# Optimization experiments

Measured on AMD Instinct MI355X. Metric: run time of the kernel, lower is better.

## Reference

```python
import jax, jax.numpy as jnp
import numpy as np

NEG = 10000.0


def setup_inputs() -> dict:
    key0 = jax.random.key(0)
    k1, k2, k3, k4 = jax.random.split(key0, 4)
    B, S, D = 4, 4096, 64
    query = jax.random.normal(k1, (B, S, D), dtype=jnp.float32)
    key = jax.random.normal(k2, (B, S, D), dtype=jnp.float32)
    value = jax.random.normal(k3, (B, S, D), dtype=jnp.float32)
    mask = jax.random.randint(k4, (B, S), 0, 2, dtype=jnp.int32)
    return {"query": query, "key": key, "value": value, "mask": mask}


def reference(query, key, value, mask):
    B, Sq, D = query.shape
    Sk = key.shape[1]
    # scaled scores: [B, Sq, Sk]
    e = jnp.einsum("bqd,bkd->bqk", query, key) / jnp.sqrt(jnp.asarray(D, query.dtype))
    # history_only (causal) additive mask: penalize positions where key idx > query idx
    causal = (jnp.arange(Sk)[None, :] > jnp.arange(Sq)[:, None]).astype(query.dtype)
    e = e - NEG * causal[None, :, :]
    # padding mask on keys: [B, 1, Sk]
    e = e - NEG * (1.0 - mask.astype(query.dtype))[:, None, :]
    attn = jax.nn.softmax(e, axis=-1)
    return jnp.einsum("bqk,bkd->bqd", attn, value)
```

## Files before the change

kernel.cpp:

```cpp
#include <hip/hip_runtime.h>

typedef __attribute__((ext_vector_type(8))) short  bf16x8;
typedef __attribute__((ext_vector_type(4))) float  f32x4;

#define S_LEN 4096
#define DH    64
#define NEGF  10000.0f

__device__ __forceinline__ unsigned short f2bf(float f) {
  unsigned u = __float_as_uint(f);
  u += 0x7FFF + ((u >> 16) & 1);
  return (unsigned short)(u >> 16);
}

__device__ __forceinline__ bf16x8 pack8(float4 a, float4 b) {
  bf16x8 r;
  r[0] = (short)f2bf(a.x); r[1] = (short)f2bf(a.y);
  r[2] = (short)f2bf(a.z); r[3] = (short)f2bf(a.w);
  r[4] = (short)f2bf(b.x); r[5] = (short)f2bf(b.y);
  r[6] = (short)f2bf(b.z); r[7] = (short)f2bf(b.w);
  return r;
}

__device__ __forceinline__ int swz(int row, int colb) {
  return (row << 7) + (colb ^ ((row & 7) << 4));
}

__global__ __launch_bounds__(1024, 1)
void attn_fwd(const float* __restrict__ Q, const float* __restrict__ K,
              const float* __restrict__ V, const int* __restrict__ Msk,
              float* __restrict__ O) {
  __shared__ __align__(16) unsigned char smem[98304];
  __shared__ int sfb;
  unsigned char* smK  = smem;
  unsigned char* smVt = smem + 32768;
  unsigned char* smP  = smem + 65536;

  const int tid  = threadIdx.x;
  const int lane = tid & 63;
  const int wid  = tid >> 6;
  const int g    = wid >> 2;
  const int r    = wid & 3;
  const int p    = lane & 15;
  const int h    = lane >> 4;

  const int b  = blockIdx.x >> 6;
  const int qt = blockIdx.x & 63;
  const int q0 = qt << 6;

  const float* Qb = Q + ((size_t)b * S_LEN) * DH;
  const float* Kb = K + ((size_t)b * S_LEN) * DH;
  const float* Vb = V + ((size_t)b * S_LEN) * DH;
  const int*   Mb = Msk + b * S_LEN;

  if (tid == 0) sfb = S_LEN;
  __syncthreads();
  {
    int loc = S_LEN;
    for (int k = tid; k < S_LEN; k += 1024)
      if (Mb[k]) { loc = k; break; }
    if (loc < S_LEN) atomicMin(&sfb, loc);
  }
  __syncthreads();
  const int fb = sfb;

  bf16x8 qf[2];
  {
    const float* qp = Qb + (size_t)(q0 + g * 16 + p) * DH + h * 8;
    const float4* q4a = (const float4*)(qp);
    const float4* q4b = (const float4*)(qp + 32);
    qf[0] = pack8(q4a[0], q4a[1]);
    qf[1] = pack8(q4b[0], q4b[1]);
  }

  f32x4 o[4];
  float m_r[4], l_r[4];
#pragma unroll
  for (int j = 0; j < 4; ++j)
#pragma unroll
    for (int e = 0; e < 4; ++e) o[j][e] = 0.f;
#pragma unroll
  for (int rr = 0; rr < 4; ++rr) { m_r[rr] = -INFINITY; l_r[rr] = 0.f; }

  const int qrb = q0 + g * 16 + h * 4;

  const int ns = (qt >> 2) + 1;
  for (int s = 0; s < ns; ++s) {
    const int kb4 = s << 2;
    __syncthreads();

#pragma unroll
    for (int cc = 0; cc < 2; ++cc) {
      const int idx = tid + (cc << 10);
      {
        const int row256 = idx >> 3;
        const int colf   = (idx & 7) << 3;
        const int t      = row256 >> 6;
        const int row    = row256 & 63;
        if (kb4 + t <= qt) {
          const float4* kp =
              (const float4*)(Kb + (size_t)((kb4 + t) * 64 + row) * DH + colf);
          float4 k0 = kp[0], k1 = kp[1];
          *(bf16x8*)(smK + t * 8192 + swz(row, colf << 1)) = pack8(k0, k1);
        }
      }
      {
        const int t2   = idx >> 9;
        const int i    = idx & 511;
        const int dcol = i & 63;
        const int kc   = i >> 6;
        if (kb4 + t2 <= qt) {
          bf16x8 vp;
#pragma unroll
          for (int e = 0; e < 8; ++e)
            vp[e] = (short)f2bf(
                Vb[(size_t)((kb4 + t2) * 64 + kc * 8 + e) * DH + dcol]);
          *(bf16x8*)(smVt + t2 * 8192 + swz(dcol, kc << 4)) = vp;
        }
      }
    }
    __syncthreads();

    const int j = kb4 + r;
    if (j <= qt) {
      const int kv0 = j << 6;
      const unsigned char* myK  = smK  + r * 8192;
      const unsigned char* myVt = smVt + r * 8192;

      f32x4 acc[4];
#pragma unroll
      for (int t16 = 0; t16 < 4; ++t16) {
        f32x4 a;
#pragma unroll
        for (int e = 0; e < 4; ++e) a[e] = 0.f;
#pragma unroll
        for (int c = 0; c < 2; ++c) {
          bf16x8 kb = *(const bf16x8*)(myK + swz(t16 * 16 + p, c * 64 + h * 16));
          a = __builtin_amdgcn_mfma_f32_16x16x32_bf16(qf[c], kb, a, 0, 0, 0);
        }
        acc[t16] = a;
      }

      float pen[4];
#pragma unroll
      for (int t16 = 0; t16 < 4; ++t16)
        pen[t16] = Mb[kv0 + t16 * 16 + p] ? 0.f : -NEGF;

      float sc[4][4];
#pragma unroll
      for (int t16 = 0; t16 < 4; ++t16) {
        const int key = kv0 + t16 * 16 + p;
#pragma unroll
        for (int rr = 0; rr < 4; ++rr) {
          float v = fmaf(acc[t16][rr], 0.125f, pen[t16]);
          if (key > qrb + rr) v -= NEGF;
          sc[t16][rr] = v;
        }
      }

      float alpha[4];
#pragma unroll
      for (int rr = 0; rr < 4; ++rr) {
        float v = fmaxf(fmaxf(sc[0][rr], sc[1][rr]), fmaxf(sc[2][rr], sc[3][rr]));
        v = fmaxf(v, __shfl_xor(v, 1));
        v = fmaxf(v, __shfl_xor(v, 2));
        v = fmaxf(v, __shfl_xor(v, 4));
        v = fmaxf(v, __shfl_xor(v, 8));
        const float mn = fmaxf(m_r[rr], v);
        alpha[rr] = __expf(m_r[rr] - mn);
        m_r[rr] = mn;
      }

      unsigned char* Pw = smP + (wid << 11);
      float rs[4] = {0.f, 0.f, 0.f, 0.f};
#pragma unroll
      for (int t16 = 0; t16 < 4; ++t16) {
#pragma unroll
        for (int rr = 0; rr < 4; ++rr) {
          float pv = __expf(sc[t16][rr] - m_r[rr]);
          rs[rr] += pv;
          *(unsigned short*)(Pw + swz(h * 4 + rr, (t16 * 16 + p) << 1)) = f2bf(pv);
        }
      }
#pragma unroll
      for (int rr = 0; rr < 4; ++rr) {
        float v = rs[rr];
        v += __shfl_xor(v, 1);
        v += __shfl_xor(v, 2);
        v += __shfl_xor(v, 4);
        v += __shfl_xor(v, 8);
        l_r[rr] = l_r[rr] * alpha[rr] + v;
      }
#pragma unroll
      for (int jj = 0; jj < 4; ++jj)
#pragma unroll
        for (int rr = 0; rr < 4; ++rr) o[jj][rr] *= alpha[rr];

      asm volatile("s_waitcnt lgkmcnt(0)" ::: "memory");
      __builtin_amdgcn_sched_barrier(0);

      bf16x8 pf[2];
#pragma unroll
      for (int c = 0; c < 2; ++c)
        pf[c] = *(const bf16x8*)(Pw + swz(p, c * 64 + h * 16));
#pragma unroll
      for (int jj = 0; jj < 4; ++jj)
#pragma unroll
        for (int c = 0; c < 2; ++c) {
          bf16x8 vb = *(const bf16x8*)(myVt + swz(jj * 16 + p, c * 64 + h * 16));
          o[jj] = __builtin_amdgcn_mfma_f32_16x16x32_bf16(pf[c], vb, o[jj], 0, 0, 0);
        }
    }
  }

  __syncthreads();
  {
    float* wb = (float*)smem + wid * 1536 + lane * 24;
#pragma unroll
    for (int rr = 0; rr < 4; ++rr) { wb[rr] = m_r[rr]; wb[4 + rr] = l_r[rr]; }
#pragma unroll
    for (int jj = 0; jj < 4; ++jj)
#pragma unroll
      for (int rr = 0; rr < 4; ++rr) wb[8 + jj * 4 + rr] = o[jj][rr];
  }
  __syncthreads();

  if (r == 0) {
    const float* b0 = (float*)smem + (wid + 0) * 1536 + lane * 24;
    const float* b1 = (float*)smem + (wid + 1) * 1536 + lane * 24;
    const float* b2 = (float*)smem + (wid + 2) * 1536 + lane * 24;
    const float* b3 = (float*)smem + (wid + 3) * 1536 + lane * 24;
    float* Ob = O + ((size_t)b * S_LEN) * DH;
#pragma unroll
    for (int rr = 0; rr < 4; ++rr) {
      if (qrb + rr < fb) continue;
      const float M = fmaxf(fmaxf(b0[rr], b1[rr]), fmaxf(b2[rr], b3[rr]));
      const float w0 = __expf(b0[rr] - M), w1 = __expf(b1[rr] - M);
      const float w2 = __expf(b2[rr] - M), w3 = __expf(b3[rr] - M);
      const float L = b0[4 + rr] * w0 + b1[4 + rr] * w1 +
                      b2[4 + rr] * w2 + b3[4 + rr] * w3;
      const float inv = 1.f / L;
#pragma unroll
      for (int jj = 0; jj < 4; ++jj) {
        const float num = b0[8 + jj * 4 + rr] * w0 + b1[8 + jj * 4 + rr] * w1 +
                          b2[8 + jj * 4 + rr] * w2 + b3[8 + jj * 4 + rr] * w3;
        Ob[(size_t)(qrb + rr) * DH + jj * 16 + p] = num * inv;
      }
    }
  }

  for (int dq = qt; dq < fb; dq += 64) {
    __syncthreads();
    float* ssc   = (float*)smem;
    float* sq    = (float*)smem + 4096;
    float* spart = (float*)smem + 4160;
    float* sred  = (float*)smem + 5184;
    if (tid < 64) sq[tid] = Qb[(size_t)dq * DH + tid];
    __syncthreads();

    float lmax = -1e30f;
    for (int k = tid; k < S_LEN; k += 1024) {
      float s = -1e30f;
      if (k <= dq || Mb[k]) {
        const float4* kp = (const float4*)(Kb + (size_t)k * DH);
        float acc = 0.f;
#pragma unroll
        for (int d4 = 0; d4 < 16; ++d4) {
          const float4 kv = kp[d4];
          acc += sq[d4 * 4 + 0] * kv.x + sq[d4 * 4 + 1] * kv.y +
                 sq[d4 * 4 + 2] * kv.z + sq[d4 * 4 + 3] * kv.w;
        }
        s = acc * 0.125f;
      }
      ssc[k] = s;
      lmax = fmaxf(lmax, s);
    }
#pragma unroll
    for (int o2 = 32; o2; o2 >>= 1) lmax = fmaxf(lmax, __shfl_xor(lmax, o2));
    if (lane == 0) sred[wid] = lmax;
    __syncthreads();
    float gmax = sred[0];
#pragma unroll
    for (int i = 1; i < 16; ++i) gmax = fmaxf(gmax, sred[i]);

    float lsum = 0.f;
    for (int k = tid; k < S_LEN; k += 1024) {
      const float e = (ssc[k] > -1e29f) ? __expf(ssc[k] - gmax) : 0.f;
      ssc[k] = e;
      lsum += e;
    }
#pragma unroll
    for (int o2 = 32; o2; o2 >>= 1) lsum += __shfl_xor(lsum, o2);
    if (lane == 0) sred[16 + wid] = lsum;
    __syncthreads();
    float gsum = 0.f;
#pragma unroll
    for (int i = 0; i < 16; ++i) gsum += sred[16 + i];
    const float inv = 1.f / gsum;

    {
      const int k0d = wid << 8;
      float a0 = 0.f, a1 = 0.f, a2 = 0.f, a3 = 0.f;
      for (int kk = 0; kk < 256; kk += 4) {
        a0 = fmaf(ssc[k0d + kk + 0], Vb[(size_t)(k0d + kk + 0) * DH + lane], a0);
        a1 = fmaf(ssc[k0d + kk + 1], Vb[(size_t)(k0d + kk + 1) * DH + lane], a1);
        a2 = fmaf(ssc[k0d + kk + 2], Vb[(size_t)(k0d + kk + 2) * DH + lane], a2);
        a3 = fmaf(ssc[k0d + kk + 3], Vb[(size_t)(k0d + kk + 3) * DH + lane], a3);
      }
      spart[wid * 64 + lane] = (a0 + a1) + (a2 + a3);
    }
    __syncthreads();
    if (tid < 64) {
      float num = 0.f;
#pragma unroll
      for (int i = 0; i < 16; ++i) num += spart[i * 64 + tid];
      O[((size_t)b * S_LEN + dq) * DH + tid] = num * inv;
    }
  }
}

extern "C" void kernel_launch(void* const* d_in, const int* in_sizes, int n_in,
                              void* d_out, int out_size, void* d_ws, size_t ws_size,
                              hipStream_t stream) {
  const float* Q = (const float*)d_in[0];
  const float* K = (const float*)d_in[1];
  const float* V = (const float*)d_in[2];
  const int*   M = (const int*)d_in[3];
  float* O = (float*)d_out;
  attn_fwd<<<dim3(4 * (S_LEN / 64)), dim3(1024), 0, stream>>>(Q, K, V, M, O);
}
```

Baseline: 146.2 us.

## Register-prefetch next K/V tile and mask during compute; transpose split-merge LDS layout

```diff
diff --git a/kernel.cpp b/kernel.cpp
--- a/kernel.cpp
+++ b/kernel.cpp
@@ -53,8 +53,65 @@
   const float* Vb = V + ((size_t)b * S_LEN) * DH;
   const int*   Mb = Msk + b * S_LEN;
 
+  const int k_row0 = tid >> 3;
+  const int k_colf = (tid & 7) << 3;
+  const int v_dcol = tid & 63;
+  const int v_kc0  = tid >> 6;
+
+  float4 pk[2][2];
+  float  pv[2][8];
+  int    pm[4];
+
+  auto PREFETCH = [&](int s) {
+    const int kb4 = s << 2;
+#pragma unroll
+    for (int cc = 0; cc < 2; ++cc) {
+      const int rr256 = k_row0 + (cc << 7);
+      const int kt = rr256 >> 6, krow = rr256 & 63;
+      if (kb4 + kt <= qt) {
+        const float4* kp =
+            (const float4*)(Kb + (size_t)((kb4 + kt) * 64 + krow) * DH + k_colf);
+        pk[cc][0] = kp[0]; pk[cc][1] = kp[1];
+      }
+      const int kc16 = v_kc0 + (cc << 4);
+      const int vt = kc16 >> 3, vkc = kc16 & 7;
+      if (kb4 + vt <= qt) {
+#pragma unroll
+        for (int e = 0; e < 8; ++e)
+          pv[cc][e] = Vb[(size_t)((kb4 + vt) * 64 + vkc * 8 + e) * DH + v_dcol];
+      }
+    }
+    const int j = kb4 + r;
+    if (j <= qt) {
+#pragma unroll
+      for (int t16 = 0; t16 < 4; ++t16)
+        pm[t16] = Mb[(j << 6) + t16 * 16 + p];
+    }
+  };
+
+  auto WRITE_LDS = [&](int s) {
+    const int kb4 = s << 2;
+#pragma unroll
+    for (int cc = 0; cc < 2; ++cc) {
+      const int rr256 = k_row0 + (cc << 7);
+      const int kt = rr256 >> 6, krow = rr256 & 63;
+      if (kb4 + kt <= qt)
+        *(bf16x8*)(smK + kt * 8192 + swz(krow, k_colf << 1)) =
+            pack8(pk[cc][0], pk[cc][1]);
+      const int kc16 = v_kc0 + (cc << 4);
+      const int vt = kc16 >> 3, vkc = kc16 & 7;
+      if (kb4 + vt <= qt) {
+        bf16x8 vp;
+#pragma unroll
+        for (int e = 0; e < 8; ++e) vp[e] = (short)f2bf(pv[cc][e]);
+        *(bf16x8*)(smVt + vt * 8192 + swz(v_dcol, vkc << 4)) = vp;
+      }
+    }
+  };
+
   if (tid == 0) sfb = S_LEN;
   __syncthreads();
+  PREFETCH(0);
   {
     int loc = S_LEN;
     for (int k = tid; k < S_LEN; k += 1024)
@@ -86,42 +143,16 @@
 
   const int ns = (qt >> 2) + 1;
   for (int s = 0; s < ns; ++s) {
-    const int kb4 = s << 2;
-    __syncthreads();
-
-#pragma unroll
-    for (int cc = 0; cc < 2; ++cc) {
-      const int idx = tid + (cc << 10);
-      {
-        const int row256 = idx >> 3;
-        const int colf   = (idx & 7) << 3;
-        const int t      = row256 >> 6;
-        const int row    = row256 & 63;
-        if (kb4 + t <= qt) {
-          const float4* kp =
-              (const float4*)(Kb + (size_t)((kb4 + t) * 64 + row) * DH + colf);
-          float4 k0 = kp[0], k1 = kp[1];
-          *(bf16x8*)(smK + t * 8192 + swz(row, colf << 1)) = pack8(k0, k1);
-        }
-      }
-      {
-        const int t2   = idx >> 9;
-        const int i    = idx & 511;
-        const int dcol = i & 63;
-        const int kc   = i >> 6;
-        if (kb4 + t2 <= qt) {
-          bf16x8 vp;
-#pragma unroll
-          for (int e = 0; e < 8; ++e)
-            vp[e] = (short)f2bf(
-                Vb[(size_t)((kb4 + t2) * 64 + kc * 8 + e) * DH + dcol]);
-          *(bf16x8*)(smVt + t2 * 8192 + swz(dcol, kc << 4)) = vp;
-        }
-      }
-    }
-    __syncthreads();
-
-    const int j = kb4 + r;
+    __syncthreads();
+    WRITE_LDS(s);
+    const int j = (s << 2) + r;
+    float pen[4];
+#pragma unroll
+    for (int t16 = 0; t16 < 4; ++t16)
+      pen[t16] = pm[t16] ? 0.f : -NEGF;
+    __syncthreads();
+    if (s + 1 < ns) PREFETCH(s + 1);
+
     if (j <= qt) {
       const int kv0 = j << 6;
       const unsigned char* myK  = smK  + r * 8192;
@@ -140,11 +171,6 @@
         }
         acc[t16] = a;
       }
-
-      float pen[4];
-#pragma unroll
-      for (int t16 = 0; t16 < 4; ++t16)
-        pen[t16] = Mb[kv0 + t16 * 16 + p] ? 0.f : -NEGF;
 
       float sc[4][4];
 #pragma unroll
@@ -177,9 +203,9 @@
       for (int t16 = 0; t16 < 4; ++t16) {
 #pragma unroll
         for (int rr = 0; rr < 4; ++rr) {
-          float pv = __expf(sc[t16][rr] - m_r[rr]);
-          rs[rr] += pv;
-          *(unsigned short*)(Pw + swz(h * 4 + rr, (t16 * 16 + p) << 1)) = f2bf(pv);
+          float pv2 = __expf(sc[t16][rr] - m_r[rr]);
+          rs[rr] += pv2;
+          *(unsigned short*)(Pw + swz(h * 4 + rr, (t16 * 16 + p) << 1)) = f2bf(pv2);
         }
       }
 #pragma unroll
@@ -215,35 +241,40 @@
 
   __syncthreads();
   {
-    float* wb = (float*)smem + wid * 1536 + lane * 24;
-#pragma unroll
-    for (int rr = 0; rr < 4; ++rr) { wb[rr] = m_r[rr]; wb[4 + rr] = l_r[rr]; }
+    float* wb = (float*)smem + wid * 64 + lane;
+#pragma unroll
+    for (int rr = 0; rr < 4; ++rr) {
+      wb[(rr)     * 1024] = m_r[rr];
+      wb[(4 + rr) * 1024] = l_r[rr];
+    }
 #pragma unroll
     for (int jj = 0; jj < 4; ++jj)
 #pragma unroll
-      for (int rr = 0; rr < 4; ++rr) wb[8 + jj * 4 + rr] = o[jj][rr];
+      for (int rr = 0; rr < 4; ++rr)
+        wb[(8 + jj * 4 + rr) * 1024] = o[jj][rr];
   }
   __syncthreads();
 
   if (r == 0) {
-    const float* b0 = (float*)smem + (wid + 0) * 1536 + lane * 24;
-    const float* b1 = (float*)smem + (wid + 1) * 1536 + lane * 24;
-    const float* b2 = (float*)smem + (wid + 2) * 1536 + lane * 24;
-    const float* b3 = (float*)smem + (wid + 3) * 1536 + lane * 24;
+    const float* w0 = (float*)smem + (wid + 0) * 64 + lane;
+    const float* w1 = (float*)smem + (wid + 1) * 64 + lane;
+    const float* w2 = (float*)smem + (wid + 2) * 64 + lane;
+    const float* w3 = (float*)smem + (wid + 3) * 64 + lane;
     float* Ob = O + ((size_t)b * S_LEN) * DH;
 #pragma unroll
     for (int rr = 0; rr < 4; ++rr) {
       if (qrb + rr < fb) continue;
-      const float M = fmaxf(fmaxf(b0[rr], b1[rr]), fmaxf(b2[rr], b3[rr]));
-      const float w0 = __expf(b0[rr] - M), w1 = __expf(b1[rr] - M);
-      const float w2 = __expf(b2[rr] - M), w3 = __expf(b3[rr] - M);
-      const float L = b0[4 + rr] * w0 + b1[4 + rr] * w1 +
-                      b2[4 + rr] * w2 + b3[4 + rr] * w3;
+      const float M = fmaxf(fmaxf(w0[rr * 1024], w1[rr * 1024]),
+                            fmaxf(w2[rr * 1024], w3[rr * 1024]));
+      const float e0 = __expf(w0[rr * 1024] - M), e1 = __expf(w1[rr * 1024] - M);
+      const float e2 = __expf(w2[rr * 1024] - M), e3 = __expf(w3[rr * 1024] - M);
+      const float L = w0[(4 + rr) * 1024] * e0 + w1[(4 + rr) * 1024] * e1 +
+                      w2[(4 + rr) * 1024] * e2 + w3[(4 + rr) * 1024] * e3;
       const float inv = 1.f / L;
 #pragma unroll
       for (int jj = 0; jj < 4; ++jj) {
-        const float num = b0[8 + jj * 4 + rr] * w0 + b1[8 + jj * 4 + rr] * w1 +
-                          b2[8 + jj * 4 + rr] * w2 + b3[8 + jj * 4 + rr] * w3;
+        const int e = (8 + jj * 4 + rr) * 1024;
+        const float num = w0[e] * e0 + w1[e] * e1 + w2[e] * e2 + w3[e] * e3;
         Ob[(size_t)(qrb + rr) * DH + jj * 16 + p] = num * inv;
       }
     }
```

Measured after the change: 173.4 us. 1.19x slower.

## Split causal attention into split-KV partial blocks plus a separate merge kernel

Applied to the files above, without the earlier changes.

```diff
diff --git a/kernel.cpp b/kernel.cpp
--- a/kernel.cpp
+++ b/kernel.cpp
@@ -6,6 +6,9 @@
 #define S_LEN 4096
 #define DH    64
 #define NEGF  10000.0f
+
+#define NSLOT   288
+#define PSTRIDE 4224
 
 __device__ __forceinline__ unsigned short f2bf(float f) {
   unsigned u = __float_as_uint(f);
@@ -26,296 +29,300 @@
   return (row << 7) + (colb ^ ((row & 7) << 4));
 }
 
-__global__ __launch_bounds__(1024, 1)
-void attn_fwd(const float* __restrict__ Q, const float* __restrict__ K,
-              const float* __restrict__ V, const int* __restrict__ Msk,
-              float* __restrict__ O) {
-  __shared__ __align__(16) unsigned char smem[98304];
+__global__ __launch_bounds__(256, 1)
+void attn_part(const float* __restrict__ Q, const float* __restrict__ K,
+               const float* __restrict__ V, const int* __restrict__ Msk,
+               float* __restrict__ O, float* __restrict__ ws) {
+  __shared__ __align__(16) unsigned char smem[24576];
   __shared__ int sfb;
   unsigned char* smK  = smem;
-  unsigned char* smVt = smem + 32768;
-  unsigned char* smP  = smem + 65536;
+  unsigned char* smVt = smem + 8192;
+  unsigned char* smP  = smem + 16384;
 
   const int tid  = threadIdx.x;
   const int lane = tid & 63;
   const int wid  = tid >> 6;
-  const int g    = wid >> 2;
-  const int r    = wid & 3;
   const int p    = lane & 15;
   const int h    = lane >> 4;
 
-  const int b  = blockIdx.x >> 6;
-  const int qt = blockIdx.x & 63;
-  const int q0 = qt << 6;
+  const int b   = blockIdx.y;
+  const int rem = blockIdx.x;
+  int g = 0;
+  while (4 * (g + 1) * (g + 2) <= rem) ++g;
+  const int off = rem - 4 * g * (g + 1);
+  const int qt  = 8 * g + off / (g + 1);
+  const int c   = off - (off / (g + 1)) * (g + 1);
+  const int q0  = qt << 6;
 
   const float* Qb = Q + ((size_t)b * S_LEN) * DH;
   const float* Kb = K + ((size_t)b * S_LEN) * DH;
   const float* Vb = V + ((size_t)b * S_LEN) * DH;
   const int*   Mb = Msk + b * S_LEN;
 
+  bf16x8 qf[2];
+  {
+    const float* qp = Qb + (size_t)(q0 + wid * 16 + p) * DH + h * 8;
+    const float4* q4a = (const float4*)(qp);
+    const float4* q4b = (const float4*)(qp + 32);
+    qf[0] = pack8(q4a[0], q4a[1]);
+    qf[1] = pack8(q4b[0], q4b[1]);
+  }
+
+  f32x4 o[4];
+  float m_r[4], l_r[4];
+#pragma unroll
+  for (int j = 0; j < 4; ++j)
+#pragma unroll
+    for (int e = 0; e < 4; ++e) o[j][e] = 0.f;
+#pragma unroll
+  for (int rr = 0; rr < 4; ++rr) { m_r[rr] = -INFINITY; l_r[rr] = 0.f; }
+
+  const int qrb = q0 + wid * 16 + h * 4;
+
+  const int j0 = c << 3;
+  const int j1 = min(j0 + 8, qt + 1);
+  for (int j = j0; j < j1; ++j) {
+    const int kv0 = j << 6;
+    __syncthreads();
+
+#pragma unroll
+    for (int cc = 0; cc < 2; ++cc) {
+      const int chunk = tid + (cc << 8);
+      const int row   = chunk >> 3;
+      const int colf  = (chunk & 7) << 3;
+      const float4* kp = (const float4*)(Kb + (size_t)(kv0 + row) * DH + colf);
+      float4 k0 = kp[0], k1 = kp[1];
+      *(bf16x8*)(smK + swz(row, colf << 1)) = pack8(k0, k1);
+
+      const int dcol = tid & 63;
+      const int kc   = (tid >> 6) + (cc << 2);
+      bf16x8 vp;
+#pragma unroll
+      for (int e = 0; e < 8; ++e)
+        vp[e] = (short)f2bf(Vb[(size_t)(kv0 + kc * 8 + e) * DH + dcol]);
+      *(bf16x8*)(smVt + swz(dcol, kc << 4)) = vp;
+    }
+    __syncthreads();
+
+    f32x4 acc[4];
+#pragma unroll
+    for (int t16 = 0; t16 < 4; ++t16) {
+      f32x4 a;
+#pragma unroll
+      for (int e = 0; e < 4; ++e) a[e] = 0.f;
+#pragma unroll
+      for (int cc = 0; cc < 2; ++cc) {
+        bf16x8 kb = *(const bf16x8*)(smK + swz(t16 * 16 + p, cc * 64 + h * 16));
+        a = __builtin_amdgcn_mfma_f32_16x16x32_bf16(qf[cc], kb, a, 0, 0, 0);
+      }
+      acc[t16] = a;
+    }
+
+    float pen[4];
+#pragma unroll
+    for (int t16 = 0; t16 < 4; ++t16)
+      pen[t16] = Mb[kv0 + t16 * 16 + p] ? 0.f : -NEGF;
+
+    float sc[4][4];
+#pragma unroll
+    for (int t16 = 0; t16 < 4; ++t16) {
+      const int key = kv0 + t16 * 16 + p;
+#pragma unroll
+      for (int rr = 0; rr < 4; ++rr) {
+        float v = fmaf(acc[t16][rr], 0.125f, pen[t16]);
+        if (key > qrb + rr) v -= NEGF;
+        sc[t16][rr] = v;
+      }
+    }
+
+    float alpha[4];
+#pragma unroll
+    for (int rr = 0; rr < 4; ++rr) {
+      float v = fmaxf(fmaxf(sc[0][rr], sc[1][rr]), fmaxf(sc[2][rr], sc[3][rr]));
+      v = fmaxf(v, __shfl_xor(v, 1));
+      v = fmaxf(v, __shfl_xor(v, 2));
+      v = fmaxf(v, __shfl_xor(v, 4));
+      v = fmaxf(v, __shfl_xor(v, 8));
+      const float mn = fmaxf(m_r[rr], v);
+      alpha[rr] = __expf(m_r[rr] - mn);
+      m_r[rr] = mn;
+    }
+
+    unsigned char* Pw = smP + (wid << 11);
+    float rs[4] = {0.f, 0.f, 0.f, 0.f};
+#pragma unroll
+    for (int t16 = 0; t16 < 4; ++t16) {
+#pragma unroll
+      for (int rr = 0; rr < 4; ++rr) {
+        float pv = __expf(sc[t16][rr] - m_r[rr]);
+        rs[rr] += pv;
+        *(unsigned short*)(Pw + swz(h * 4 + rr, (t16 * 16 + p) << 1)) = f2bf(pv);
+      }
+    }
+#pragma unroll
+    for (int rr = 0; rr < 4; ++rr) {
+      float v = rs[rr];
+      v += __shfl_xor(v, 1);
+      v += __shfl_xor(v, 2);
+      v += __shfl_xor(v, 4);
+      v += __shfl_xor(v, 8);
+      l_r[rr] = l_r[rr] * alpha[rr] + v;
+    }
+#pragma unroll
+    for (int jj = 0; jj < 4; ++jj)
+#pragma unroll
+      for (int rr = 0; rr < 4; ++rr) o[jj][rr] *= alpha[rr];
+
+    asm volatile("s_waitcnt lgkmcnt(0)" ::: "memory");
+    __builtin_amdgcn_sched_barrier(0);
+
+    bf16x8 pf[2];
+#pragma unroll
+    for (int cc = 0; cc < 2; ++cc)
+      pf[cc] = *(const bf16x8*)(Pw + swz(p, cc * 64 + h * 16));
+#pragma unroll
+    for (int jj = 0; jj < 4; ++jj)
+#pragma unroll
+      for (int cc = 0; cc < 2; ++cc) {
+        bf16x8 vb = *(const bf16x8*)(smVt + swz(jj * 16 + p, cc * 64 + h * 16));
+        o[jj] = __builtin_amdgcn_mfma_f32_16x16x32_bf16(pf[cc], vb, o[jj], 0, 0, 0);
+      }
+  }
+
+  {
+    float* W = ws + (size_t)(b * NSLOT + rem) * PSTRIDE;
+#pragma unroll
+    for (int rr = 0; rr < 4; ++rr) {
+      const int ql = wid * 16 + h * 4 + rr;
+      if (p == 0) { W[ql] = m_r[rr]; W[64 + ql] = l_r[rr]; }
+#pragma unroll
+      for (int jj = 0; jj < 4; ++jj)
+        W[128 + ql * 64 + jj * 16 + p] = o[jj][rr];
+    }
+  }
+
+  if (c == 0) {
+    if (tid == 0) sfb = S_LEN;
+    __syncthreads();
+    {
+      int loc = S_LEN;
+      for (int k = tid; k < S_LEN; k += 256)
+        if (Mb[k]) { loc = k; break; }
+      if (loc < S_LEN) atomicMin(&sfb, loc);
+    }
+    __syncthreads();
+    const int fb = sfb;
+
+    for (int dq = qt; dq < fb; dq += 64) {
+      __syncthreads();
+      float* ssc   = (float*)smem;
+      float* sq    = (float*)smem + 4096;
+      float* sred  = (float*)smem + 4160;
+      float* spart = (float*)smem + 4224;
+      if (tid < 64) sq[tid] = Qb[(size_t)dq * DH + tid];
+      __syncthreads();
+
+      float lmax = -1e30f;
+      for (int k = tid; k < S_LEN; k += 256) {
+        float s = -1e30f;
+        if (k <= dq || Mb[k]) {
+          const float4* kp = (const float4*)(Kb + (size_t)k * DH);
+          float acc2 = 0.f;
+#pragma unroll
+          for (int d4 = 0; d4 < 16; ++d4) {
+            const float4 kv = kp[d4];
+            acc2 += sq[d4 * 4 + 0] * kv.x + sq[d4 * 4 + 1] * kv.y +
+                    sq[d4 * 4 + 2] * kv.z + sq[d4 * 4 + 3] * kv.w;
+          }
+          s = acc2 * 0.125f;
+        }
+        ssc[k] = s;
+        lmax = fmaxf(lmax, s);
+      }
+#pragma unroll
+      for (int o2 = 32; o2; o2 >>= 1) lmax = fmaxf(lmax, __shfl_xor(lmax, o2));
+      if (lane == 0) sred[wid] = lmax;
+      __syncthreads();
+      const float gmax = fmaxf(fmaxf(sred[0], sred[1]), fmaxf(sred[2], sred[3]));
+
+      float lsum = 0.f;
+      for (int k = tid; k < S_LEN; k += 256) {
+        const float e = (ssc[k] > -1e29f) ? __expf(ssc[k] - gmax) : 0.f;
+        ssc[k] = e;
+        lsum += e;
+      }
+#pragma unroll
+      for (int o2 = 32; o2; o2 >>= 1) lsum += __shfl_xor(lsum, o2);
+      if (lane == 0) sred[4 + wid] = lsum;
+      __syncthreads();
+      const float inv = 1.f / (sred[4] + sred[5] + sred[6] + sred[7]);
+
+      {
+        const int k0d = wid << 10;
+        float a0 = 0.f, a1 = 0.f;
+        for (int kk = 0; kk < 1024; kk += 2) {
+          a0 = fmaf(ssc[k0d + kk + 0], Vb[(size_t)(k0d + kk + 0) * DH + lane], a0);
+          a1 = fmaf(ssc[k0d + kk + 1], Vb[(size_t)(k0d + kk + 1) * DH + lane], a1);
+        }
+        spart[wid * 64 + lane] = a0 + a1;
+      }
+      __syncthreads();
+      if (tid < 64) {
+        const float num = spart[tid] + spart[64 + tid] + spart[128 + tid] +
+                          spart[192 + tid];
+        O[((size_t)b * S_LEN + dq) * DH + tid] = num * inv;
+      }
+    }
+  }
+}
+
+__global__ __launch_bounds__(256, 1)
+void attn_merge(const int* __restrict__ Msk, const float* __restrict__ ws,
+                float* __restrict__ O) {
+  __shared__ int sfb;
+  const int tid = threadIdx.x;
+  const int qt = blockIdx.x, b = blockIdx.y;
+  const int g = qt >> 3;
+  const int base = (g + 1) * (qt - 4 * g);
+  const int Nc = g + 1;
+  const int*   Mb = Msk + b * S_LEN;
+
   if (tid == 0) sfb = S_LEN;
   __syncthreads();
   {
     int loc = S_LEN;
-    for (int k = tid; k < S_LEN; k += 1024)
+    for (int k = tid; k < S_LEN; k += 256)
       if (Mb[k]) { loc = k; break; }
     if (loc < S_LEN) atomicMin(&sfb, loc);
   }
   __syncthreads();
   const int fb = sfb;
 
-  bf16x8 qf[2];
-  {
-    const float* qp = Qb + (size_t)(q0 + g * 16 + p) * DH + h * 8;
-    const float4* q4a = (const float4*)(qp);
-    const float4* q4b = (const float4*)(qp + 32);
-    qf[0] = pack8(q4a[0], q4a[1]);
-    qf[1] = pack8(q4b[0], q4b[1]);
-  }
-
-  f32x4 o[4];
-  float m_r[4], l_r[4];
-#pragma unroll
-  for (int j = 0; j < 4; ++j)
-#pragma unroll
-    for (int e = 0; e < 4; ++e) o[j][e] = 0.f;
-#pragma unroll
-  for (int rr = 0; rr < 4; ++rr) { m_r[rr] = -INFINITY; l_r[rr] = 0.f; }
-
-  const int qrb = q0 + g * 16 + h * 4;
-
-  const int ns = (qt >> 2) + 1;
-  for (int s = 0; s < ns; ++s) {
-    const int kb4 = s << 2;
-    __syncthreads();
-
-#pragma unroll
-    for (int cc = 0; cc < 2; ++cc) {
-      const int idx = tid + (cc << 10);
-      {
-        const int row256 = idx >> 3;
-        const int colf   = (idx & 7) << 3;
-        const int t      = row256 >> 6;
-        const int row    = row256 & 63;
-        if (kb4 + t <= qt) {
-          const float4* kp =
-              (const float4*)(Kb + (size_t)((kb4 + t) * 64 + row) * DH + colf);
-          float4 k0 = kp[0], k1 = kp[1];
-          *(bf16x8*)(smK + t * 8192 + swz(row, colf << 1)) = pack8(k0, k1);
-        }
-      }
-      {
-        const int t2   = idx >> 9;
-        const int i    = idx & 511;
-        const int dcol = i & 63;
-        const int kc   = i >> 6;
-        if (kb4 + t2 <= qt) {
-          bf16x8 vp;
-#pragma unroll
-          for (int e = 0; e < 8; ++e)
-            vp[e] = (short)f2bf(
-                Vb[(size_t)((kb4 + t2) * 64 + kc * 8 + e) * DH + dcol]);
-          *(bf16x8*)(smVt + t2 * 8192 + swz(dcol, kc << 4)) = vp;
-        }
-      }
-    }
-    __syncthreads();
-
-    const int j = kb4 + r;
-    if (j <= qt) {
-      const int kv0 = j << 6;
-      const unsigned char* myK  = smK  + r * 8192;
-      const unsigned char* myVt = smVt + r * 8192;
-
-      f32x4 acc[4];
-#pragma unroll
-      for (int t16 = 0; t16 < 4; ++t16) {
-        f32x4 a;
-#pragma unroll
-        for (int e = 0; e < 4; ++e) a[e] = 0.f;
-#pragma unroll
-        for (int c = 0; c < 2; ++c) {
-          bf16x8 kb = *(const bf16x8*)(myK + swz(t16 * 16 + p, c * 64 + h * 16));
-          a = __builtin_amdgcn_mfma_f32_16x16x32_bf16(qf[c], kb, a, 0, 0, 0);
-        }
-        acc[t16] = a;
-      }
-
-      float pen[4];
-#pragma unroll
-      for (int t16 = 0; t16 < 4; ++t16)
-        pen[t16] = Mb[kv0 + t16 * 16 + p] ? 0.f : -NEGF;
-
-      float sc[4][4];
-#pragma unroll
-      for (int t16 = 0; t16 < 4; ++t16) {
-        const int key = kv0 + t16 * 16 + p;
-#pragma unroll
-        for (int rr = 0; rr < 4; ++rr) {
-          float v = fmaf(acc[t16][rr], 0.125f, pen[t16]);
-          if (key > qrb + rr) v -= NEGF;
-          sc[t16][rr] = v;
-        }
-      }
-
-      float alpha[4];
-#pragma unroll
-      for (int rr = 0; rr < 4; ++rr) {
-        float v = fmaxf(fmaxf(sc[0][rr], sc[1][rr]), fmaxf(sc[2][rr], sc[3][rr]));
-        v = fmaxf(v, __shfl_xor(v, 1));
-        v = fmaxf(v, __shfl_xor(v, 2));
-        v = fmaxf(v, __shfl_xor(v, 4));
-        v = fmaxf(v, __shfl_xor(v, 8));
-        const float mn = fmaxf(m_r[rr], v);
-        alpha[rr] = __expf(m_r[rr] - mn);
-        m_r[rr] = mn;
-      }
-
-      unsigned char* Pw = smP + (wid << 11);
-      float rs[4] = {0.f, 0.f, 0.f, 0.f};
-#pragma unroll
-      for (int t16 = 0; t16 < 4; ++t16) {
-#pragma unroll
-        for (int rr = 0; rr < 4; ++rr) {
-          float pv = __expf(sc[t16][rr] - m_r[rr]);
-          rs[rr] += pv;
-          *(unsigned short*)(Pw + swz(h * 4 + rr, (t16 * 16 + p) << 1)) = f2bf(pv);
-        }
-      }
-#pragma unroll
-      for (int rr = 0; rr < 4; ++rr) {
-        float v = rs[rr];
-        v += __shfl_xor(v, 1);
-        v += __shfl_xor(v, 2);
-        v += __shfl_xor(v, 4);
-        v += __shfl_xor(v, 8);
-        l_r[rr] = l_r[rr] * alpha[rr] + v;
-      }
-#pragma unroll
-      for (int jj = 0; jj < 4; ++jj)
-#pragma unroll
-        for (int rr = 0; rr < 4; ++rr) o[jj][rr] *= alpha[rr];
-
-      asm volatile("s_waitcnt lgkmcnt(0)" ::: "memory");
-      __builtin_amdgcn_sched_barrier(0);
-
-      bf16x8 pf[2];
-#pragma unroll
-      for (int c = 0; c < 2; ++c)
-        pf[c] = *(const bf16x8*)(Pw + swz(p, c * 64 + h * 16));
-#pragma unroll
-      for (int jj = 0; jj < 4; ++jj)
-#pragma unroll
-        for (int c = 0; c < 2; ++c) {
-          bf16x8 vb = *(const bf16x8*)(myVt + swz(jj * 16 + p, c * 64 + h * 16));
-          o[jj] = __builtin_amdgcn_mfma_f32_16x16x32_bf16(pf[c], vb, o[jj], 0, 0, 0);
-        }
-    }
-  }
-
-  __syncthreads();
-  {
-    float* wb = (float*)smem + wid * 1536 + lane * 24;
-#pragma unroll
-    for (int rr = 0; rr < 4; ++rr) { wb[rr] = m_r[rr]; wb[4 + rr] = l_r[rr]; }
-#pragma unroll
-    for (int jj = 0; jj < 4; ++jj)
-#pragma unroll
-      for (int rr = 0; rr < 4; ++rr) wb[8 + jj * 4 + rr] = o[jj][rr];
-  }
-  __syncthreads();
-
-  if (r == 0) {
-    const float* b0 = (float*)smem + (wid + 0) * 1536 + lane * 24;
-    const float* b1 = (float*)smem + (wid + 1) * 1536 + lane * 24;
-    const float* b2 = (float*)smem + (wid + 2) * 1536 + lane * 24;
-    const float* b3 = (float*)smem + (wid + 3) * 1536 + lane * 24;
-    float* Ob = O + ((size_t)b * S_LEN) * DH;
-#pragma unroll
-    for (int rr = 0; rr < 4; ++rr) {
-      if (qrb + rr < fb) continue;
-      const float M = fmaxf(fmaxf(b0[rr], b1[rr]), fmaxf(b2[rr], b3[rr]));
-      const float w0 = __expf(b0[rr] - M), w1 = __expf(b1[rr] - M);
-      const float w2 = __expf(b2[rr] - M), w3 = __expf(b3[rr] - M);
-      const float L = b0[4 + rr] * w0 + b1[4 + rr] * w1 +
-                      b2[4 + rr] * w2 + b3[4 + rr] * w3;
-      const float inv = 1.f / L;
-#pragma unroll
-      for (int jj = 0; jj < 4; ++jj) {
-        const float num = b0[8 + jj * 4 + rr] * w0 + b1[8 + jj * 4 + rr] * w1 +
-                          b2[8 + jj * 4 + rr] * w2 + b3[8 + jj * 4 + rr] * w3;
-        Ob[(size_t)(qrb + rr) * DH + jj * 16 + p] = num * inv;
-      }
-    }
-  }
-
-  for (int dq = qt; dq < fb; dq += 64) {
-    __syncthreads();
-    float* ssc   = (float*)smem;
-    float* sq    = (float*)smem + 4096;
-    float* spart = (float*)smem + 4160;
-    float* sred  = (float*)smem + 5184;
-    if (tid < 64) sq[tid] = Qb[(size_t)dq * DH + tid];
-    __syncthreads();
-
-    float lmax = -1e30f;
-    for (int k = tid; k < S_LEN; k += 1024) {
-      float s = -1e30f;
-      if (k <= dq || Mb[k]) {
-        const float4* kp = (const float4*)(Kb + (size_t)k * DH);
-        float acc = 0.f;
-#pragma unroll
-        for (int d4 = 0; d4 < 16; ++d4) {
-          const float4 kv = kp[d4];
-          acc += sq[d4 * 4 + 0] * kv.x + sq[d4 * 4 + 1] * kv.y +
-                 sq[d4 * 4 + 2] * kv.z + sq[d4 * 4 + 3] * kv.w;
-        }
-        s = acc * 0.125f;
-      }
-      ssc[k] = s;
-      lmax = fmaxf(lmax, s);
-    }
-#pragma unroll
-    for (int o2 = 32; o2; o2 >>= 1) lmax = fmaxf(lmax, __shfl_xor(lmax, o2));
-    if (lane == 0) sred[wid] = lmax;
-    __syncthreads();
-    float gmax = sred[0];
-#pragma unroll
-    for (int i = 1; i < 16; ++i) gmax = fmaxf(gmax, sred[i]);
-
-    float lsum = 0.f;
-    for (int k = tid; k < S_LEN; k += 1024) {
-      const float e = (ssc[k] > -1e29f) ? __expf(ssc[k] - gmax) : 0.f;
-      ssc[k] = e;
-      lsum += e;
-    }
-#pragma unroll
-    for (int o2 = 32; o2; o2 >>= 1) lsum += __shfl_xor(lsum, o2);
-    if (lane == 0) sred[16 + wid] = lsum;
-    __syncthreads();
-    float gsum = 0.f;
-#pragma unroll
-    for (int i = 0; i < 16; ++i) gsum += sred[16 + i];
-    const float inv = 1.f / gsum;
-
-    {
-      const int k0d = wid << 8;
-      float a0 = 0.f, a1 = 0.f, a2 = 0.f, a3 = 0.f;
-      for (int kk = 0; kk < 256; kk += 4) {
-        a0 = fmaf(ssc[k0d + kk + 0], Vb[(size_t)(k0d + kk + 0) * DH + lane], a0);
-        a1 = fmaf(ssc[k0d + kk + 1], Vb[(size_t)(k0d + kk + 1) * DH + lane], a1);
-        a2 = fmaf(ssc[k0d + kk + 2], Vb[(size_t)(k0d + kk + 2) * DH + lane], a2);
-        a3 = fmaf(ssc[k0d + kk + 3], Vb[(size_t)(k0d + kk + 3) * DH + lane], a3);
-      }
-      spart[wid * 64 + lane] = (a0 + a1) + (a2 + a3);
-    }
-    __syncthreads();
-    if (tid < 64) {
-      float num = 0.f;
-#pragma unroll
-      for (int i = 0; i < 16; ++i) num += spart[i * 64 + tid];
-      O[((size_t)b * S_LEN + dq) * DH + tid] = num * inv;
-    }
+  const int ql = tid >> 2;
+  const int cg = tid & 3;
+  const int q  = (qt << 6) + ql;
+  if (q < fb) return;
+
+  const float* P0 = ws + (size_t)(b * NSLOT + base) * PSTRIDE;
+
+  float M = -INFINITY;
+  for (int cc = 0; cc < Nc; ++cc) M = fmaxf(M, P0[(size_t)cc * PSTRIDE + ql]);
+  float w[8];
+  float L = 0.f;
+  for (int cc = 0; cc < Nc; ++cc) {
+    w[cc] = __expf(P0[(size_t)cc * PSTRIDE + ql] - M);
+    L += P0[(size_t)cc * PSTRIDE + 64 + ql] * w[cc];
+  }
+  const float inv = 1.f / L;
+
+  float* Ob = O + ((size_t)b * S_LEN + q) * DH;
+#pragma unroll 4
+  for (int e = 0; e < 16; ++e) {
+    const int col = cg * 16 + e;
+    float num = 0.f;
+    for (int cc = 0; cc < Nc; ++cc)
+      num += P0[(size_t)cc * PSTRIDE + 128 + ql * 64 + col] * w[cc];
+    Ob[col] = num * inv;
   }
 }
 
@@ -327,5 +334,13 @@
   const float* V = (const float*)d_in[2];
   const int*   M = (const int*)d_in[3];
   float* O = (float*)d_out;
-  attn_fwd<<<dim3(4 * (S_LEN / 64)), dim3(1024), 0, stream>>>(Q, K, V, M, O);
-}
+  float* ws = (float*)d_ws;
+  const size_t need = (size_t)4 * NSLOT * PSTRIDE * sizeof(float);
+  if (ws_size >= need) {
+    attn_part<<<dim3(NSLOT, 4), dim3(256), 0, stream>>>(Q, K, V, M, O, ws);
+    attn_merge<<<dim3(64, 4), dim3(256), 0, stream>>>(M, ws, O);
+  } else {
+    attn_part<<<dim3(NSLOT, 4), dim3(256), 0, stream>>>(Q, K, V, M, O, ws);
+    attn_merge<<<dim3(64, 4), dim3(256), 0, stream>>>(M, ws, O);
+  }
+}
```

Result: slower. 169.6 us (+16.0%).
